# Optimization experiments

Hardware: AMD Instinct MI355X
Metric: run time of the kernel (lower is better)

## Reference

```python
import jax, jax.numpy as jnp
import numpy as np

ATTN_MASK_VALUE = -1e10
N = 8192
DIM = 1024
DIM_HEAD = 64
DIM_OUT = 1024

def setup_inputs() -> dict:
    key = jax.random.key(0)
    k1, k2, k3 = jax.random.split(key, 3)
    x = jax.random.normal(k1, (N, DIM), dtype=jnp.float32)
    Wqkv = jax.random.normal(k2, (DIM, 3 * DIM_HEAD), dtype=jnp.float32) * (DIM ** -0.5)
    Wout = jax.random.normal(k3, (DIM_HEAD, DIM_OUT), dtype=jnp.float32) * (DIM_HEAD ** -0.5)
    bout = jnp.zeros((DIM_OUT,), dtype=jnp.float32)
    return {"x": x, "Wqkv": Wqkv, "Wout": Wout, "bout": bout}

def reference(x, Wqkv, Wout, bout) -> jnp.ndarray:
    n = x.shape[0]
    scale = DIM_HEAD ** -0.5
    qkv = x @ Wqkv                      # [n, 3*dh]
    q, k, v = jnp.split(qkv, 3, axis=-1)  # each [n, dh]
    sim = jnp.einsum('id,jd->ij', q, k) * scale  # [n, n]
    mask = jnp.tril(jnp.ones((n, n), dtype=bool))
    sim = jnp.where(mask, sim, ATTN_MASK_VALUE)
    attn = jax.nn.softmax(sim, axis=-1)
    out = jnp.einsum('ij,jd->id', attn, v)  # [n, dh]
    return out @ Wout + bout            # [n, dim_out]
```

## Files before the change

### kernel.cpp

```cpp
#include <hip/hip_runtime.h>
#include <hip/hip_bf16.h>

#define N_TOK 8192

typedef float f32x4  __attribute__((ext_vector_type(4)));
typedef float f32x16 __attribute__((ext_vector_type(16)));
typedef short bf16x8 __attribute__((ext_vector_type(8)));
typedef unsigned int u32x4 __attribute__((ext_vector_type(4)));

__device__ inline short f2bf(float f) {
    union { __hip_bfloat16 h; short s; } u;
    u.h = __float2bfloat16(f);
    return u.s;
}
__device__ inline unsigned cvtpk(float lo, float hi) {
    unsigned r;
    asm("v_cvt_pk_bf16_f32 %0, %1, %2" : "=v"(r) : "v"(lo), "v"(hi));
    return r;
}
__device__ inline void plswap(unsigned &a, unsigned &b) {
    asm("v_permlane32_swap_b32 %0, %1" : "+v"(a), "+v"(b));
}

#define PREC 2080


__global__ __launch_bounds__(256) void conv_kernel(
    const float* __restrict__ Wqkv,
    const float* __restrict__ Wout,
    __hip_bfloat16* __restrict__ Wt,
    __hip_bfloat16* __restrict__ WoT) {
    __shared__ float tile[32][33];
    const int t = threadIdx.x;
    const int cc = t & 31, rbase = t >> 5;
    const int b = blockIdx.x;
    if (b < 192) {
        const int r0 = (b & 31) * 32;
        const int c0 = (b >> 5) * 32;
        #pragma unroll
        for (int it = 0; it < 4; ++it) {
            const int rr = rbase + it * 8;
            tile[rr][cc] = Wqkv[(size_t)(r0 + rr) * 192 + c0 + cc];
        }
        __syncthreads();
        #pragma unroll
        for (int it = 0; it < 4; ++it) {
            const int rr = rbase + it * 8;
            Wt[(size_t)(c0 + rr) * 1024 + r0 + cc] = __float2bfloat16(tile[cc][rr]);
        }
    } else {
        const int bb = b - 192;
        const int r0 = (bb & 1) * 32;
        const int c0 = (bb >> 1) * 32;
        #pragma unroll
        for (int it = 0; it < 4; ++it) {
            const int rr = rbase + it * 8;
            tile[rr][cc] = Wout[(size_t)(r0 + rr) * 1024 + c0 + cc];
        }
        __syncthreads();
        #pragma unroll
        for (int it = 0; it < 4; ++it) {
            const int rr = rbase + it * 8;
            WoT[(size_t)(c0 + rr) * 64 + r0 + cc] = __float2bfloat16(tile[cc][rr]);
        }
    }
}

__global__ __launch_bounds__(256) void qkv_kernel(
    const float* __restrict__ x,
    const __hip_bfloat16* __restrict__ Wt,
    __hip_bfloat16* __restrict__ Qf,
    __hip_bfloat16* __restrict__ Kf,
    __hip_bfloat16* __restrict__ Vf) {
    __shared__ __hip_bfloat16 sA[2][16 * 64];
    __shared__ __hip_bfloat16 sB[2][192 * 64];
    __shared__ __hip_bfloat16 sV[64][20];
    const int tid = threadIdx.x;
    const int w = tid >> 6, lane = tid & 63;
    const int l16 = lane & 15, lq = lane >> 4;
    const int m0 = blockIdx.x * 16;

    const int ar = tid >> 4;
    const int ac = (tid & 15) >> 1;
    const int ah = tid & 1;
    const float* agp = x + (size_t)(m0 + ar) * 1024 + ac * 8 + ah * 4;
    const int aoff = ar * 64 + ((ac ^ (ar & 7)) * 8) + ah * 4;

    int boff[6];
    const __hip_bfloat16* bgp[6];
    #pragma unroll
    for (int i = 0; i < 6; ++i) {
        const int q = i * 256 + tid;
        const int r = q >> 3, c = q & 7;
        bgp[i] = Wt + (size_t)r * 1024 + c * 8;
        boff[i] = r * 64 + ((c ^ (r & 7)) * 8);
    }

    const int arow = l16;
    const int aswz0 = arow * 64 + ((lq ^ (arow & 7)) * 8);
    const int aswz1 = arow * 64 + (((4 + lq) ^ (arow & 7)) * 8);
    int bswz0[3], bswz1[3];
    #pragma unroll
    for (int j = 0; j < 3; ++j) {
        const int row = (w * 3 + j) * 16 + l16;
        bswz0[j] = row * 64 + ((lq ^ (row & 7)) * 8);
        bswz1[j] = row * 64 + (((4 + lq) ^ (row & 7)) * 8);
    }

    f32x4 acc[3];
    #pragma unroll
    for (int j = 0; j < 3; ++j) acc[j] = (f32x4)0.f;

    float4 areg;
    u32x4 breg[6];

    areg = *reinterpret_cast<const float4*>(agp);
    #pragma unroll
    for (int i = 0; i < 6; ++i)
        breg[i] = *reinterpret_cast<const u32x4*>(bgp[i]);
    {
        uint2 aw; aw.x = cvtpk(areg.x, areg.y); aw.y = cvtpk(areg.z, areg.w);
        *reinterpret_cast<uint2*>(&sA[0][aoff]) = aw;
        #pragma unroll
        for (int i = 0; i < 6; ++i)
            *reinterpret_cast<u32x4*>(&sB[0][boff[i]]) = breg[i];
    }
    __syncthreads();

    for (int ks = 0; ks < 16; ++ks) {
        const int cur = ks & 1;
        if (ks < 15) {
            areg = *reinterpret_cast<const float4*>(agp + (ks + 1) * 64);
            #pragma unroll
            for (int i = 0; i < 6; ++i)
                breg[i] = *reinterpret_cast<const u32x4*>(bgp[i] + (ks + 1) * 64);
        }
        bf16x8 af0 = *reinterpret_cast<const bf16x8*>(&sA[cur][aswz0]);
        bf16x8 af1 = *reinterpret_cast<const bf16x8*>(&sA[cur][aswz1]);
        #pragma unroll
        for (int j = 0; j < 3; ++j) {
            bf16x8 b0 = *reinterpret_cast<const bf16x8*>(&sB[cur][bswz0[j]]);
            bf16x8 b1 = *reinterpret_cast<const bf16x8*>(&sB[cur][bswz1[j]]);
            acc[j] = __builtin_amdgcn_mfma_f32_16x16x32_bf16(b0, af0, acc[j], 0, 0, 0);
            acc[j] = __builtin_amdgcn_mfma_f32_16x16x32_bf16(b1, af1, acc[j], 0, 0, 0);
        }
        if (ks < 15) {
            uint2 aw; aw.x = cvtpk(areg.x, areg.y); aw.y = cvtpk(areg.z, areg.w);
            *reinterpret_cast<uint2*>(&sA[cur ^ 1][aoff]) = aw;
            #pragma unroll
            for (int i = 0; i < 6; ++i)
                *reinterpret_cast<u32x4*>(&sB[cur ^ 1][boff[i]]) = breg[i];
        }
        __syncthreads();
    }

    const int row = m0 + l16;
    #pragma unroll
    for (int j = 0; j < 3; ++j) {
        const int nt = w * 3 + j;
        const int nb = nt * 16 + 4 * lq;
        if (nt < 4) {
            const int tq = row >> 5, lr = row & 31;
            const int kc = nb >> 4, hi2 = (nb >> 3) & 1, jj = nb & 7;
            short4 qs;
            qs.x = f2bf(acc[j][0] * 0.18033688011112042f);
            qs.y = f2bf(acc[j][1] * 0.18033688011112042f);
            qs.z = f2bf(acc[j][2] * 0.18033688011112042f);
            qs.w = f2bf(acc[j][3] * 0.18033688011112042f);
            *reinterpret_cast<short4*>(Qf + ((size_t)(tq * 4 + kc) * 64 + lr + 32 * hi2) * 8 + jj) = qs;
        } else if (nt < 8) {
            const int col = nb - 64;
            const int c = row >> 6, rr = row & 63, hk = rr >> 5, lr = rr & 31;
            const int kc = col >> 4, hi2 = (col >> 3) & 1, jj = col & 7;
            short4 ks4;
            ks4.x = f2bf(acc[j][0]); ks4.y = f2bf(acc[j][1]);
            ks4.z = f2bf(acc[j][2]); ks4.w = f2bf(acc[j][3]);
            *reinterpret_cast<short4*>(Kf + ((size_t)(c * 8 + 4 * hk + kc) * 64 + lr + 32 * hi2) * 8 + jj) = ks4;
        } else {
            #pragma unroll
            for (int r = 0; r < 4; ++r)
                sV[nb + r - 128][l16] = __float2bfloat16(acc[j][r]);
        }
    }
    __syncthreads();
    const int vd = tid >> 2, vm = (tid & 3) * 4;
    short4 vv = *reinterpret_cast<const short4*>(&sV[vd][vm]);
    const int kv = m0 + vm;
    const int c = kv >> 6, ks2 = (kv >> 4) & 3, hi2 = (kv >> 3) & 1, jj = kv & 7;
    *reinterpret_cast<short4*>(Vf + ((size_t)(c * 8 + 4 * (vd >> 5) + ks2) * 64 + (vd & 31) + 32 * hi2) * 8 + jj) = vv;
}

__global__ __launch_bounds__(512, 2) void attn_kernel(
    const __hip_bfloat16* __restrict__ Qf,
    const __hip_bfloat16* __restrict__ Kf,
    const __hip_bfloat16* __restrict__ Vf,
    float* __restrict__ Part) {
    __shared__ float sO[8][64][32];
    __shared__ float sL[8][32];
    const int tid = threadIdx.x;
    const int w = tid >> 6, lane = tid & 63;
    const int l31 = lane & 31, hi = lane >> 5;
    const int p = blockIdx.x >> 2, s = blockIdx.x & 3;
    const int slot = w * 4 + s;

    for (int ti = 0; ti < 2; ++ti) {
        const int t = ti ? (255 - p) : p;
        const int q0 = t * 32;
        const int Ct = (q0 + 95) >> 6;
        const int qabs = q0 + l31;

        bf16x8 qf[4];
        #pragma unroll
        for (int kc = 0; kc < 4; ++kc)
            qf[kc] = *reinterpret_cast<const bf16x8*>(
                Qf + ((size_t)(t * 4 + kc) * 64 + lane) * 8);

        float l = 0.f;
        f32x16 Oa = (f32x16)0.f, Oc = (f32x16)0.f;

        if (slot < Ct) {
            bf16x8 ka0[4], kb0[4], va0[4], vb0[4];
            bf16x8 ka1[4], kb1[4], va1[4], vb1[4];

            auto LOADCHUNK = [&](bf16x8* kA, bf16x8* kB, bf16x8* vA,
                                 bf16x8* vB, int cc) {
                const __hip_bfloat16* kp = Kf + (size_t)cc * 4096 + lane * 8;
                const __hip_bfloat16* vp = Vf + (size_t)cc * 4096 + lane * 8;
                #pragma unroll
                for (int kc = 0; kc < 4; ++kc) {
                    kA[kc] = *reinterpret_cast<const bf16x8*>(kp + kc * 512);
                    kB[kc] = *reinterpret_cast<const bf16x8*>(kp + 2048 + kc * 512);
                    vA[kc] = *reinterpret_cast<const bf16x8*>(vp + kc * 512);
                    vB[kc] = *reinterpret_cast<const bf16x8*>(vp + 2048 + kc * 512);
                }
            };

            auto PROCESS = [&](int cc, const bf16x8* kA, const bf16x8* kB,
                               const bf16x8* vA, const bf16x8* vB) {
                const int kv0 = cc * 64;
                f32x16 Sa = (f32x16)(-16.f), Sb = (f32x16)(-16.f);
                #pragma unroll
                for (int kc = 0; kc < 4; ++kc)
                    Sa = __builtin_amdgcn_mfma_f32_32x32x16_bf16(kA[kc], qf[kc], Sa, 0, 0, 0);
                #pragma unroll
                for (int kc = 0; kc < 4; ++kc)
                    Sb = __builtin_amdgcn_mfma_f32_32x32x16_bf16(kB[kc], qf[kc], Sb, 0, 0, 0);

                if (kv0 + 64 > q0) {
                    #pragma unroll
                    for (int r = 0; r < 16; ++r) {
                        const int rowk = (r & 3) + 8 * (r >> 2) + 4 * hi;
                        if (kv0 + rowk > qabs)      Sa[r] = -1.0e30f;
                        if (kv0 + 32 + rowk > qabs) Sb[r] = -1.0e30f;
                    }
                }

                #pragma unroll
                for (int r = 0; r < 16; ++r) Sa[r] = exp2f(Sa[r]);
                #pragma unroll
                for (int r = 0; r < 16; ++r) Sb[r] = exp2f(Sb[r]);
                float s8[8];
                #pragma unroll
                for (int j = 0; j < 8; ++j)
                    s8[j] = (Sa[2*j] + Sa[2*j+1]) + (Sb[2*j] + Sb[2*j+1]);
                #pragma unroll
                for (int j = 0; j < 4; ++j) s8[j] += s8[j+4];
                float ps = (s8[0] + s8[2]) + (s8[1] + s8[3]);
                ps += __shfl_xor(ps, 32);
                l += ps;

                bf16x8 F0, F1, F2, F3;
                {
                    unsigned a0 = cvtpk(Sa[0], Sa[1]),  a1 = cvtpk(Sa[2], Sa[3]);
                    unsigned a2 = cvtpk(Sa[4], Sa[5]),  a3 = cvtpk(Sa[6], Sa[7]);
                    plswap(a0, a2); plswap(a1, a3);
                    u32x4 w0; w0[0]=a0; w0[1]=a1; w0[2]=a2; w0[3]=a3;
                    F0 = __builtin_bit_cast(bf16x8, w0);
                    unsigned b0 = cvtpk(Sa[8], Sa[9]),  b1 = cvtpk(Sa[10], Sa[11]);
                    unsigned b2 = cvtpk(Sa[12], Sa[13]), b3 = cvtpk(Sa[14], Sa[15]);
                    plswap(b0, b2); plswap(b1, b3);
                    u32x4 w1; w1[0]=b0; w1[1]=b1; w1[2]=b2; w1[3]=b3;
                    F1 = __builtin_bit_cast(bf16x8, w1);
                    unsigned c0_ = cvtpk(Sb[0], Sb[1]),  c1_ = cvtpk(Sb[2], Sb[3]);
                    unsigned c2_ = cvtpk(Sb[4], Sb[5]),  c3_ = cvtpk(Sb[6], Sb[7]);
                    plswap(c0_, c2_); plswap(c1_, c3_);
                    u32x4 w2; w2[0]=c0_; w2[1]=c1_; w2[2]=c2_; w2[3]=c3_;
                    F2 = __builtin_bit_cast(bf16x8, w2);
                    unsigned d0 = cvtpk(Sb[8], Sb[9]),  d1 = cvtpk(Sb[10], Sb[11]);
                    unsigned d2 = cvtpk(Sb[12], Sb[13]), d3 = cvtpk(Sb[14], Sb[15]);
                    plswap(d0, d2); plswap(d1, d3);
                    u32x4 w3; w3[0]=d0; w3[1]=d1; w3[2]=d2; w3[3]=d3;
                    F3 = __builtin_bit_cast(bf16x8, w3);
                }
                bf16x8 Fa[4] = {F0, F1, F2, F3};
                #pragma unroll
                for (int ks = 0; ks < 4; ++ks) {
                    Oa = __builtin_amdgcn_mfma_f32_32x32x16_bf16(vA[ks], Fa[ks], Oa, 0, 0, 0);
                    Oc = __builtin_amdgcn_mfma_f32_32x32x16_bf16(vB[ks], Fa[ks], Oc, 0, 0, 0);
                }
            };

            LOADCHUNK(ka0, kb0, va0, vb0, slot);
            for (int c = slot; c < Ct; c += 64) {
                if (c + 32 < Ct) LOADCHUNK(ka1, kb1, va1, vb1, c + 32);
                PROCESS(c, ka0, kb0, va0, vb0);
                if (c + 64 < Ct) LOADCHUNK(ka0, kb0, va0, vb0, c + 64);
                if (c + 32 < Ct) PROCESS(c + 32, ka1, kb1, va1, vb1);
            }
        }

        if (hi == 0) sL[w][l31] = l;
        #pragma unroll
        for (int r = 0; r < 16; ++r) {
            const int d = (r & 3) + 8 * (r >> 2) + 4 * hi;
            sO[w][d][l31]      = Oa[r];
            sO[w][d + 32][l31] = Oc[r];
        }
        __syncthreads();

        float* pb = Part + (size_t)(t * 4 + s) * PREC;
        for (int e = tid; e < 2048; e += 512) {
            const int d = e >> 5, qq = e & 31;
            float ob = 0.f;
            #pragma unroll
            for (int wi = 0; wi < 8; ++wi) ob += sO[wi][d][qq];
            pb[e] = ob;
            if (d == 0) {
                float lb = 0.f;
                #pragma unroll
                for (int wi = 0; wi < 8; ++wi) lb += sL[wi][qq];
                pb[2048 + qq] = lb;
            }
        }
        __syncthreads();
    }
}

__global__ __launch_bounds__(256) void merge_kernel(
    const float* __restrict__ Part, __hip_bfloat16* __restrict__ Ob) {
    const int t = blockIdx.x, q0 = t * 32;
    const float* pp = Part + (size_t)(t * 4) * PREC;
    for (int e = threadIdx.x; e < 2048; e += 256) {
        const int qq = e & 31, d = e >> 5;
        float ll = 0.f, oo = 0.f;
        #pragma unroll
        for (int si = 0; si < 4; ++si) {
            ll += pp[si * PREC + 2048 + qq];
            oo += pp[si * PREC + d * 32 + qq];
        }
        Ob[(size_t)(q0 + qq) * 64 + d] = __float2bfloat16(oo / ll);
    }
}

__global__ __launch_bounds__(256) void out_kernel(
    const __hip_bfloat16* __restrict__ Ob,
    const __hip_bfloat16* __restrict__ WoT,
    const float* __restrict__ bout,
    float* __restrict__ out) {
    const int tid = threadIdx.x;
    const int w = tid >> 6, lane = tid & 63;
    const int l16 = lane & 15, lq = lane >> 4;
    const int m0 = blockIdx.x * 64 + w * 16;
    const int n0 = blockIdx.y * 256;

    const __hip_bfloat16* orow = Ob + (size_t)(m0 + l16) * 64;
    bf16x8 a0 = *reinterpret_cast<const bf16x8*>(orow + 8 * lq);
    bf16x8 a1 = *reinterpret_cast<const bf16x8*>(orow + 32 + 8 * lq);

    const int row = m0 + l16;
    for (int nt = 0; nt < 16; ++nt) {
        const __hip_bfloat16* wrow = WoT + (size_t)(n0 + nt * 16 + l16) * 64;
        bf16x8 b0 = *reinterpret_cast<const bf16x8*>(wrow + 8 * lq);
        bf16x8 b1 = *reinterpret_cast<const bf16x8*>(wrow + 32 + 8 * lq);
        f32x4 acc = (f32x4)0.f;
        acc = __builtin_amdgcn_mfma_f32_16x16x32_bf16(b0, a0, acc, 0, 0, 0);
        acc = __builtin_amdgcn_mfma_f32_16x16x32_bf16(b1, a1, acc, 0, 0, 0);
        const int nb = n0 + nt * 16 + 4 * lq;
        float4 bb = *reinterpret_cast<const float4*>(bout + nb);
        float4 res;
        res.x = acc[0] + bb.x; res.y = acc[1] + bb.y;
        res.z = acc[2] + bb.z; res.w = acc[3] + bb.w;
        *reinterpret_cast<float4*>(out + (size_t)row * 1024 + nb) = res;
    }
}

extern "C" void kernel_launch(void* const* d_in, const int* in_sizes, int n_in,
                              void* d_out, int out_size, void* d_ws, size_t ws_size,
                              hipStream_t stream) {
    const float* x    = (const float*)d_in[0];
    const float* Wqkv = (const float*)d_in[1];
    const float* Wout = (const float*)d_in[2];
    const float* bout = (const float*)d_in[3];
    float* out = (float*)d_out;

    char* ws = (char*)d_ws;
    __hip_bfloat16* Wt  = (__hip_bfloat16*)(ws);
    __hip_bfloat16* WoT = (__hip_bfloat16*)(ws + 393216);
    __hip_bfloat16* Qf  = (__hip_bfloat16*)(ws + 524288);
    __hip_bfloat16* Kf  = (__hip_bfloat16*)(ws + 1572864);
    __hip_bfloat16* Vf  = (__hip_bfloat16*)(ws + 2621440);
    __hip_bfloat16* Ob  = (__hip_bfloat16*)(ws + 3670016);
    float*          Part = (float*)(ws + 4718592);

    conv_kernel<<<256, 256, 0, stream>>>(Wqkv, Wout, Wt, WoT);
    qkv_kernel<<<512, 256, 0, stream>>>(x, Wt, Qf, Kf, Vf);
    attn_kernel<<<512, 512, 0, stream>>>(Qf, Kf, Vf, Part);
    merge_kernel<<<256, 256, 0, stream>>>(Part, Ob);
    out_kernel<<<dim3(128, 4), 256, 0, stream>>>(Ob, WoT, bout, out);
}
```

Baseline: 78.19 us.

## Share K/V chunks across query tiles via LDS with async global-to-LDS loads

The attention kernel is reorganised so each block covers four 32-row query tiles (a 128-row group), and each wave handles one query tile and one 32-key half of a chunk. K and V chunks are staged into double-buffered LDS with global_load_lds, so one global read feeds several query tiles. Before, every wave loaded K/V straight into registers. Partials are now stored per (tile, split, half) as bf16 outputs normalised by their own row sum, plus the sum, and the merge kernel reweights them across 16 records. The change trades more partial records and a bf16 rounding of partials for less global K/V traffic, fewer registers (launch bounds raised to 4 blocks) and a cross-wave LDS reduction removed from the attention kernel.

```diff
diff --git a/kernel.cpp b/kernel.cpp
--- a/kernel.cpp
+++ b/kernel.cpp
@@ -2,6 +2,7 @@
 #include <hip/hip_bf16.h>
 
 #define N_TOK 8192
+#define RREC 4352
 
 typedef float f32x4  __attribute__((ext_vector_type(4)));
 typedef float f32x16 __attribute__((ext_vector_type(16)));
@@ -21,8 +22,11 @@
 __device__ inline void plswap(unsigned &a, unsigned &b) {
     asm("v_permlane32_swap_b32 %0, %1" : "+v"(a), "+v"(b));
 }
-
-#define PREC 2080
+__device__ inline void gload_lds16(const __hip_bfloat16* g, __hip_bfloat16* s) {
+    __builtin_amdgcn_global_load_lds(
+        (const __attribute__((address_space(1))) void*)(g),
+        (__attribute__((address_space(3))) void*)(s), 16, 0, 0);
+}
 
 
 __global__ __launch_bounds__(256) void conv_kernel(
@@ -190,163 +194,132 @@
     *reinterpret_cast<short4*>(Vf + ((size_t)(c * 8 + 4 * (vd >> 5) + ks2) * 64 + (vd & 31) + 32 * hi2) * 8 + jj) = vv;
 }
 
-__global__ __launch_bounds__(512, 2) void attn_kernel(
+__global__ __launch_bounds__(512, 4) void attn_kernel(
     const __hip_bfloat16* __restrict__ Qf,
     const __hip_bfloat16* __restrict__ Kf,
     const __hip_bfloat16* __restrict__ Vf,
-    float* __restrict__ Part) {
-    __shared__ float sO[8][64][32];
-    __shared__ float sL[8][32];
+    char* __restrict__ Part) {
+    __shared__ __hip_bfloat16 sK[2][4096];
+    __shared__ __hip_bfloat16 sV2[2][4096];
     const int tid = threadIdx.x;
     const int w = tid >> 6, lane = tid & 63;
     const int l31 = lane & 31, hi = lane >> 5;
-    const int p = blockIdx.x >> 2, s = blockIdx.x & 3;
-    const int slot = w * 4 + s;
-
-    for (int ti = 0; ti < 2; ++ti) {
-        const int t = ti ? (255 - p) : p;
-        const int q0 = t * 32;
-        const int Ct = (q0 + 95) >> 6;
-        const int qabs = q0 + l31;
-
-        bf16x8 qf[4];
-        #pragma unroll
-        for (int kc = 0; kc < 4; ++kc)
-            qf[kc] = *reinterpret_cast<const bf16x8*>(
-                Qf + ((size_t)(t * 4 + kc) * 64 + lane) * 8);
-
-        float l = 0.f;
-        f32x16 Oa = (f32x16)0.f, Oc = (f32x16)0.f;
-
-        if (slot < Ct) {
-            bf16x8 ka0[4], kb0[4], va0[4], vb0[4];
-            bf16x8 ka1[4], kb1[4], va1[4], vb1[4];
-
-            auto LOADCHUNK = [&](bf16x8* kA, bf16x8* kB, bf16x8* vA,
-                                 bf16x8* vB, int cc) {
-                const __hip_bfloat16* kp = Kf + (size_t)cc * 4096 + lane * 8;
-                const __hip_bfloat16* vp = Vf + (size_t)cc * 4096 + lane * 8;
+    const int bid = blockIdx.x;
+    const int qb = (bid < 256) ? (63 - (bid >> 3)) : ((bid - 256) >> 3);
+    const int s = bid & 7;
+    const int tsub = w >> 1, h = w & 1;
+    const int tq = qb * 4 + tsub;
+    const int q0 = tq * 32;
+    const int qabs = q0 + l31;
+    const int CtB = 2 * qb + 2;
+    const int nst = (CtB > s) ? ((CtB - s + 7) >> 3) : 0;
+
+    bf16x8 qf[4];
+    #pragma unroll
+    for (int kc = 0; kc < 4; ++kc)
+        qf[kc] = *reinterpret_cast<const bf16x8*>(
+            Qf + ((size_t)(tq * 4 + kc) * 64 + lane) * 8);
+
+    float l = 0.f;
+    f32x16 Oa = (f32x16)0.f, Oc = (f32x16)0.f;
+
+    const size_t gofs = (size_t)w * 512 + lane * 8;
+
+    if (nst > 0) gload_lds16(Kf + (size_t)s * 4096 + gofs, &sK[0][w * 512]),
+                 gload_lds16(Vf + (size_t)s * 4096 + gofs, &sV2[0][w * 512]);
+    __syncthreads();
+
+    int cur = 0;
+    for (int st = 0; st < nst; ++st) {
+        const int c = s + st * 8;
+        if (st + 1 < nst) {
+            gload_lds16(Kf + (size_t)(c + 8) * 4096 + gofs, &sK[cur ^ 1][w * 512]);
+            gload_lds16(Vf + (size_t)(c + 8) * 4096 + gofs, &sV2[cur ^ 1][w * 512]);
+        }
+
+        const int kv0h = c * 64 + h * 32;
+        if (kv0h <= q0 + 31) {
+            f32x16 Sa = (f32x16)(-16.f);
+            #pragma unroll
+            for (int kc = 0; kc < 4; ++kc) {
+                bf16x8 ka = *reinterpret_cast<const bf16x8*>(
+                    &sK[cur][((4 * h + kc) * 64 + lane) * 8]);
+                Sa = __builtin_amdgcn_mfma_f32_32x32x16_bf16(ka, qf[kc], Sa, 0, 0, 0);
+            }
+
+            if (kv0h + 32 > q0) {
                 #pragma unroll
-                for (int kc = 0; kc < 4; ++kc) {
-                    kA[kc] = *reinterpret_cast<const bf16x8*>(kp + kc * 512);
-                    kB[kc] = *reinterpret_cast<const bf16x8*>(kp + 2048 + kc * 512);
-                    vA[kc] = *reinterpret_cast<const bf16x8*>(vp + kc * 512);
-                    vB[kc] = *reinterpret_cast<const bf16x8*>(vp + 2048 + kc * 512);
+                for (int r = 0; r < 16; ++r) {
+                    const int rowk = (r & 3) + 8 * (r >> 2) + 4 * hi;
+                    if (kv0h + rowk > qabs) Sa[r] = -1.0e30f;
                 }
-            };
-
-            auto PROCESS = [&](int cc, const bf16x8* kA, const bf16x8* kB,
-                               const bf16x8* vA, const bf16x8* vB) {
-                const int kv0 = cc * 64;
-                f32x16 Sa = (f32x16)(-16.f), Sb = (f32x16)(-16.f);
-                #pragma unroll
-                for (int kc = 0; kc < 4; ++kc)
-                    Sa = __builtin_amdgcn_mfma_f32_32x32x16_bf16(kA[kc], qf[kc], Sa, 0, 0, 0);
-                #pragma unroll
-                for (int kc = 0; kc < 4; ++kc)
-                    Sb = __builtin_amdgcn_mfma_f32_32x32x16_bf16(kB[kc], qf[kc], Sb, 0, 0, 0);
-
-                if (kv0 + 64 > q0) {
-                    #pragma unroll
-                    for (int r = 0; r < 16; ++r) {
-                        const int rowk = (r & 3) + 8 * (r >> 2) + 4 * hi;
-                        if (kv0 + rowk > qabs)      Sa[r] = -1.0e30f;
-                        if (kv0 + 32 + rowk > qabs) Sb[r] = -1.0e30f;
-                    }
-                }
-
-                #pragma unroll
-                for (int r = 0; r < 16; ++r) Sa[r] = exp2f(Sa[r]);
-                #pragma unroll
-                for (int r = 0; r < 16; ++r) Sb[r] = exp2f(Sb[r]);
-                float s8[8];
-                #pragma unroll
-                for (int j = 0; j < 8; ++j)
-                    s8[j] = (Sa[2*j] + Sa[2*j+1]) + (Sb[2*j] + Sb[2*j+1]);
-                #pragma unroll
-                for (int j = 0; j < 4; ++j) s8[j] += s8[j+4];
-                float ps = (s8[0] + s8[2]) + (s8[1] + s8[3]);
-                ps += __shfl_xor(ps, 32);
-                l += ps;
-
-                bf16x8 F0, F1, F2, F3;
-                {
-                    unsigned a0 = cvtpk(Sa[0], Sa[1]),  a1 = cvtpk(Sa[2], Sa[3]);
-                    unsigned a2 = cvtpk(Sa[4], Sa[5]),  a3 = cvtpk(Sa[6], Sa[7]);
-                    plswap(a0, a2); plswap(a1, a3);
-                    u32x4 w0; w0[0]=a0; w0[1]=a1; w0[2]=a2; w0[3]=a3;
-                    F0 = __builtin_bit_cast(bf16x8, w0);
-                    unsigned b0 = cvtpk(Sa[8], Sa[9]),  b1 = cvtpk(Sa[10], Sa[11]);
-                    unsigned b2 = cvtpk(Sa[12], Sa[13]), b3 = cvtpk(Sa[14], Sa[15]);
-                    plswap(b0, b2); plswap(b1, b3);
-                    u32x4 w1; w1[0]=b0; w1[1]=b1; w1[2]=b2; w1[3]=b3;
-                    F1 = __builtin_bit_cast(bf16x8, w1);
-                    unsigned c0_ = cvtpk(Sb[0], Sb[1]),  c1_ = cvtpk(Sb[2], Sb[3]);
-                    unsigned c2_ = cvtpk(Sb[4], Sb[5]),  c3_ = cvtpk(Sb[6], Sb[7]);
-                    plswap(c0_, c2_); plswap(c1_, c3_);
-                    u32x4 w2; w2[0]=c0_; w2[1]=c1_; w2[2]=c2_; w2[3]=c3_;
-                    F2 = __builtin_bit_cast(bf16x8, w2);
-                    unsigned d0 = cvtpk(Sb[8], Sb[9]),  d1 = cvtpk(Sb[10], Sb[11]);
-                    unsigned d2 = cvtpk(Sb[12], Sb[13]), d3 = cvtpk(Sb[14], Sb[15]);
-                    plswap(d0, d2); plswap(d1, d3);
-                    u32x4 w3; w3[0]=d0; w3[1]=d1; w3[2]=d2; w3[3]=d3;
-                    F3 = __builtin_bit_cast(bf16x8, w3);
-                }
-                bf16x8 Fa[4] = {F0, F1, F2, F3};
-                #pragma unroll
-                for (int ks = 0; ks < 4; ++ks) {
-                    Oa = __builtin_amdgcn_mfma_f32_32x32x16_bf16(vA[ks], Fa[ks], Oa, 0, 0, 0);
-                    Oc = __builtin_amdgcn_mfma_f32_32x32x16_bf16(vB[ks], Fa[ks], Oc, 0, 0, 0);
-                }
-            };
-
-            LOADCHUNK(ka0, kb0, va0, vb0, slot);
-            for (int c = slot; c < Ct; c += 64) {
-                if (c + 32 < Ct) LOADCHUNK(ka1, kb1, va1, vb1, c + 32);
-                PROCESS(c, ka0, kb0, va0, vb0);
-                if (c + 64 < Ct) LOADCHUNK(ka0, kb0, va0, vb0, c + 64);
-                if (c + 32 < Ct) PROCESS(c + 32, ka1, kb1, va1, vb1);
             }
-        }
-
-        if (hi == 0) sL[w][l31] = l;
-        #pragma unroll
-        for (int r = 0; r < 16; ++r) {
-            const int d = (r & 3) + 8 * (r >> 2) + 4 * hi;
-            sO[w][d][l31]      = Oa[r];
-            sO[w][d + 32][l31] = Oc[r];
-        }
+
+            #pragma unroll
+            for (int r = 0; r < 16; ++r) Sa[r] = exp2f(Sa[r]);
+            float s8[8];
+            #pragma unroll
+            for (int j = 0; j < 8; ++j) s8[j] = Sa[2 * j] + Sa[2 * j + 1];
+            #pragma unroll
+            for (int j = 0; j < 4; ++j) s8[j] += s8[j + 4];
+            float ps = (s8[0] + s8[2]) + (s8[1] + s8[3]);
+            ps += __shfl_xor(ps, 32);
+            l += ps;
+
+            bf16x8 F0, F1;
+            {
+                unsigned a0 = cvtpk(Sa[0], Sa[1]),  a1 = cvtpk(Sa[2], Sa[3]);
+                unsigned a2 = cvtpk(Sa[4], Sa[5]),  a3 = cvtpk(Sa[6], Sa[7]);
+                plswap(a0, a2); plswap(a1, a3);
+                u32x4 w0; w0[0] = a0; w0[1] = a1; w0[2] = a2; w0[3] = a3;
+                F0 = __builtin_bit_cast(bf16x8, w0);
+                unsigned b0 = cvtpk(Sa[8], Sa[9]),  b1 = cvtpk(Sa[10], Sa[11]);
+                unsigned b2 = cvtpk(Sa[12], Sa[13]), b3 = cvtpk(Sa[14], Sa[15]);
+                plswap(b0, b2); plswap(b1, b3);
+                u32x4 w1; w1[0] = b0; w1[1] = b1; w1[2] = b2; w1[3] = b3;
+                F1 = __builtin_bit_cast(bf16x8, w1);
+            }
+            #pragma unroll
+            for (int ks = 0; ks < 2; ++ks) {
+                bf16x8 Fk = ks ? F1 : F0;
+                bf16x8 v0 = *reinterpret_cast<const bf16x8*>(
+                    &sV2[cur][((2 * h + ks) * 64 + lane) * 8]);
+                bf16x8 v1 = *reinterpret_cast<const bf16x8*>(
+                    &sV2[cur][((4 + 2 * h + ks) * 64 + lane) * 8]);
+                Oa = __builtin_amdgcn_mfma_f32_32x32x16_bf16(v0, Fk, Oa, 0, 0, 0);
+                Oc = __builtin_amdgcn_mfma_f32_32x32x16_bf16(v1, Fk, Oc, 0, 0, 0);
+            }
+        }
+
         __syncthreads();
-
-        float* pb = Part + (size_t)(t * 4 + s) * PREC;
-        for (int e = tid; e < 2048; e += 512) {
-            const int d = e >> 5, qq = e & 31;
-            float ob = 0.f;
-            #pragma unroll
-            for (int wi = 0; wi < 8; ++wi) ob += sO[wi][d][qq];
-            pb[e] = ob;
-            if (d == 0) {
-                float lb = 0.f;
-                #pragma unroll
-                for (int wi = 0; wi < 8; ++wi) lb += sL[wi][qq];
-                pb[2048 + qq] = lb;
-            }
-        }
-        __syncthreads();
-    }
+        cur ^= 1;
+    }
+
+    char* rec = Part + ((size_t)tq * 16 + s * 2 + h) * RREC;
+    __hip_bfloat16* On = (__hip_bfloat16*)rec;
+    const float invl = (l > 0.f) ? (1.0f / l) : 0.f;
+    #pragma unroll
+    for (int r = 0; r < 16; ++r) {
+        const int d = (r & 3) + 8 * (r >> 2) + 4 * hi;
+        On[d * 32 + l31]        = __float2bfloat16(Oa[r] * invl);
+        On[(d + 32) * 32 + l31] = __float2bfloat16(Oc[r] * invl);
+    }
+    if (hi == 0) ((float*)(rec + 4096))[l31] = l;
 }
 
 __global__ __launch_bounds__(256) void merge_kernel(
-    const float* __restrict__ Part, __hip_bfloat16* __restrict__ Ob) {
+    const char* __restrict__ Part, __hip_bfloat16* __restrict__ Ob) {
     const int t = blockIdx.x, q0 = t * 32;
-    const float* pp = Part + (size_t)(t * 4) * PREC;
+    const char* base = Part + (size_t)t * 16 * RREC;
     for (int e = threadIdx.x; e < 2048; e += 256) {
         const int qq = e & 31, d = e >> 5;
         float ll = 0.f, oo = 0.f;
         #pragma unroll
-        for (int si = 0; si < 4; ++si) {
-            ll += pp[si * PREC + 2048 + qq];
-            oo += pp[si * PREC + d * 32 + qq];
+        for (int rid = 0; rid < 16; ++rid) {
+            const char* rec = base + rid * RREC;
+            const float ls = ((const float*)(rec + 4096))[qq];
+            ll += ls;
+            oo += ls * __bfloat162float(((const __hip_bfloat16*)rec)[d * 32 + qq]);
         }
         Ob[(size_t)(q0 + qq) * 64 + d] = __float2bfloat16(oo / ll);
     }
@@ -400,7 +373,7 @@
     __hip_bfloat16* Kf  = (__hip_bfloat16*)(ws + 1572864);
     __hip_bfloat16* Vf  = (__hip_bfloat16*)(ws + 2621440);
     __hip_bfloat16* Ob  = (__hip_bfloat16*)(ws + 3670016);
-    float*          Part = (float*)(ws + 4718592);
+    char*           Part = ws + 4718592;
 
     conv_kernel<<<256, 256, 0, stream>>>(Wqkv, Wout, Wt, WoT);
     qkv_kernel<<<512, 256, 0, stream>>>(x, Wt, Qf, Kf, Vf);
```

Result: faster. 69.68 us (-10.9%).
